# Performance work log

Measured on AMD Instinct MI355X. Metric: run time of the kernel, lower is better.

Reference implementation:

```python
import jax, jax.numpy as jnp
import numpy as np

N_NODES = 100000
N_EDGES = 3200000
DIMS = [9, 18, 54, 108]


def setup_inputs() -> dict:
    key = jax.random.key(0)
    ks = jax.random.split(key, 10)
    inp = {
        "x": jax.random.normal(ks[0], (N_NODES, DIMS[0]), dtype=jnp.float32),
        "edge_index": jax.random.randint(ks[1], (2, N_EDGES), 0, N_NODES, dtype=jnp.int64),
        "edge_weight": jax.random.uniform(ks[2], (N_EDGES,), dtype=jnp.float32),
    }
    # Glorot-ish init for GCN weights, zero bias (PyG default bias init is zeros)
    for i in range(3):
        fan_in, fan_out = DIMS[i], DIMS[i + 1]
        s = (6.0 / (fan_in + fan_out)) ** 0.5
        inp[f"W{i+1}"] = jax.random.uniform(ks[3 + i], (fan_in, fan_out), jnp.float32, -s, s)
        inp[f"b{i+1}"] = jnp.zeros((fan_out,), dtype=jnp.float32)
    return inp


def _gcn_norm(edge_index, edge_weight, n_nodes):
    # Add self loops with weight 1, then symmetric normalization (PyG gcn_norm).
    loop = jnp.arange(n_nodes, dtype=edge_index.dtype)
    src = jnp.concatenate([edge_index[0], loop])
    dst = jnp.concatenate([edge_index[1], loop])
    w = jnp.concatenate([edge_weight, jnp.ones((n_nodes,), edge_weight.dtype)])
    deg = jax.ops.segment_sum(w, dst, num_segments=n_nodes)  # [N]
    dis = jnp.where(deg > 0, jax.lax.rsqrt(jnp.where(deg > 0, deg, 1.0)), 0.0)
    norm = dis[src] * w * dis[dst]  # [E+N]
    return src, dst, norm


def _gcn_layer(x, W, b, src, dst, norm, n_nodes):
    h = x @ W                              # [N, out] small GEMM
    msg = h[src] * norm[:, None]           # gather + scale  [E+N, out]
    out = jax.ops.segment_sum(msg, dst, num_segments=n_nodes)  # scatter-add
    return out + b


def reference(x, edge_index, edge_weight, W1, b1, W2, b2, W3, b3):
    n = x.shape[0]
    src, dst, norm = _gcn_norm(edge_index, edge_weight, n)
    h = jax.nn.relu(_gcn_layer(x, W1, b1, src, dst, norm, n))
    h = jax.nn.relu(_gcn_layer(h, W2, b2, src, dst, norm, n))
    h = jax.nn.relu(_gcn_layer(h, W3, b3, src, dst, norm, n))
    return h
```

## Files before the change

kernel.cpp:

```cpp
#include <hip/hip_runtime.h>
#include <hip/hip_fp16.h>

#define NN 100000
#define NE 3200000
#define NB 391
#define BCAP 9216
#define EPB 8192

static inline int cdiv(long long a, int b) { return (int)((a + b - 1) / b); }

__global__ __launch_bounds__(1024) void k_scatterB(
    const int* __restrict__ dst, const int* __restrict__ src, const float* __restrict__ w,
    int* __restrict__ bsize, int2* __restrict__ barr) {
    __shared__ int hcnt[NB];
    __shared__ int hbase[NB];
    int t = threadIdx.x;
    for (int b = t; b < NB; b += 1024) hcnt[b] = 0;
    __syncthreads();
    int base = blockIdx.x * EPB;
    int cd[8];
#pragma unroll
    for (int k = 0; k < 8; ++k) {
        int e = base + t + (k << 10);
        cd[k] = (e < NE) ? dst[e] : -1;
        if (cd[k] >= 0) atomicAdd(&hcnt[cd[k] >> 8], 1);
    }
    __syncthreads();
    for (int b = t; b < NB; b += 1024) {
        int c = hcnt[b];
        hbase[b] = (c > 0) ? atomicAdd(&bsize[b], c) : 0;
    }
    __syncthreads();
    for (int b = t; b < NB; b += 1024) hcnt[b] = 0;
    __syncthreads();
#pragma unroll
    for (int k = 0; k < 8; ++k) {
        int e = base + t + (k << 10);
        if (cd[k] >= 0) {
            int d = cd[k];
            int bk = d >> 8;
            int rk = atomicAdd(&hcnt[bk], 1);
            int pos = hbase[bk] + rk;
            if (pos < BCAP) {
                int key = ((d & 255) << 17) | src[e];
                barr[(size_t)bk * BCAP + pos] = make_int2(key, __float_as_int(w[e]));
            }
        }
    }
}

__global__ void k_scanBB(const int* __restrict__ bsize, int* __restrict__ bbase) {
    __shared__ int s[512];
    int t = threadIdx.x;
    int v = (t < NB) ? bsize[t] : 0;
    s[t] = v;
    __syncthreads();
    for (int d = 1; d < 512; d <<= 1) {
        int a = (t >= d) ? s[t - d] : 0;
        __syncthreads();
        s[t] += a;
        __syncthreads();
    }
    if (t < NB) bbase[t] = s[t] - v;
}

__global__ __launch_bounds__(256) void k_bucketCSR(
    const int2* __restrict__ barr, const int* __restrict__ bsize, const int* __restrict__ bbase,
    int* __restrict__ rowptr, float* __restrict__ dis, unsigned int* __restrict__ e2,
    const float* __restrict__ x, __half* __restrict__ y1) {
    __shared__ int cnt[256];
    __shared__ float wsum[256];
    __shared__ int rbase[256];
    __shared__ int sc[256];
    int b = blockIdx.x;
    int t = threadIdx.x;
    int nE = bsize[b];
    int ebase = bbase[b];
    const int2* rec = barr + (size_t)b * BCAP;
    cnt[t] = 0;
    wsum[t] = 0.0f;
    __syncthreads();
    for (int e = t; e < nE; e += 256) {
        int2 r = rec[e];
        int dl = (r.x >> 17) & 255;
        atomicAdd(&cnt[dl], 1);
        atomicAdd(&wsum[dl], __int_as_float(r.y));
    }
    __syncthreads();
    int v = cnt[t];
    sc[t] = v;
    __syncthreads();
    for (int d = 1; d < 256; d <<= 1) {
        int a = (t >= d) ? sc[t - d] : 0;
        __syncthreads();
        sc[t] += a;
        __syncthreads();
    }
    rbase[t] = sc[t] - v;
    int node = (b << 8) + t;
    float disv = rsqrtf(1.0f + wsum[t]);
    if (node < NN) {
        rowptr[node] = ebase + rbase[t];
        dis[node] = disv;
    }
    if (node == NN) rowptr[NN] = ebase + rbase[t];
    cnt[t] = 0;
    wsum[t] = disv;
    __syncthreads();
    for (int e = t; e < nE; e += 256) {
        int2 r = rec[e];
        int dl = (r.x >> 17) & 255;
        int rk = atomicAdd(&cnt[dl], 1);
        float wv = __int_as_float(r.y);
        int q = (int)(wv * 32768.0f + 0.5f);
        q = (q > 32767) ? 32767 : q;
        e2[(size_t)(ebase + rbase[dl] + rk)] = ((unsigned int)(r.x & 0x1FFFF) << 15) | (unsigned int)q;
    }
    int nbase = b << 8;
#pragma unroll
    for (int k = 0; k < 9; ++k) {
        int idx = (k << 8) + t;
        if (idx < 2304) {
            int nl = idx / 9;
            int f = idx - nl * 9;
            int nd = nbase + nl;
            if (nd < NN)
                y1[(size_t)nd * 16 + f] = __float2half(x[(size_t)nd * 9 + f] * wsum[nl]);
        }
    }
}

template <int F, int FPL, int YS>
__global__ void k_agg3h(const __half* __restrict__ yin, const float* __restrict__ dis,
                        const int* __restrict__ rowptr, const unsigned int* __restrict__ e2,
                        float* __restrict__ agg, int n) {
    constexpr int LPN = F / FPL;
    constexpr int NPW = 64 / LPN;
    int wv = threadIdx.x >> 6;
    int l = threadIdx.x & 63;
    int ni = l / LPN;
    int sub = l - ni * LPN;
    if (ni >= NPW) return;
    int i = (blockIdx.x * 4 + wv) * NPW + ni;
    if (i >= n) return;

    float acc0, acc1;
    if (FPL == 2) {
        __half2 hs = *(const __half2*)(yin + (size_t)i * YS + sub * 2);
        acc0 = __low2float(hs);
        acc1 = __high2float(hs);
    } else {
        acc0 = __half2float(yin[(size_t)i * YS + sub]);
        acc1 = 0.0f;
    }

    int e0 = rowptr[i];
    int e1 = rowptr[i + 1];
    int e = e0;
    const float QS = 1.0f / 32768.0f;
    for (; e + 8 <= e1; e += 8) {
        unsigned int r[8];
#pragma unroll
        for (int k = 0; k < 8; ++k) r[k] = e2[e + k];
        if (FPL == 2) {
            __half2 h[8];
#pragma unroll
            for (int k = 0; k < 8; ++k)
                h[k] = *(const __half2*)(yin + (size_t)(r[k] >> 15) * YS + sub * 2);
#pragma unroll
            for (int k = 0; k < 8; ++k) {
                float wq = (float)(r[k] & 32767u) * QS;
                acc0 = fmaf(__low2float(h[k]), wq, acc0);
                acc1 = fmaf(__high2float(h[k]), wq, acc1);
            }
        } else {
            float hv[8];
#pragma unroll
            for (int k = 0; k < 8; ++k)
                hv[k] = __half2float(yin[(size_t)(r[k] >> 15) * YS + sub]);
#pragma unroll
            for (int k = 0; k < 8; ++k) {
                float wq = (float)(r[k] & 32767u) * QS;
                acc0 = fmaf(hv[k], wq, acc0);
            }
        }
    }
    for (; e < e1; ++e) {
        unsigned int r = e2[e];
        float wq = (float)(r & 32767u) * QS;
        if (FPL == 2) {
            __half2 h = *(const __half2*)(yin + (size_t)(r >> 15) * YS + sub * 2);
            acc0 = fmaf(__low2float(h), wq, acc0);
            acc1 = fmaf(__high2float(h), wq, acc1);
        } else {
            acc0 = fmaf(__half2float(yin[(size_t)(r >> 15) * YS + sub]), wq, acc0);
        }
    }

    float di = dis[i];
    float* orow = agg + (size_t)i * F + sub * FPL;
    if (FPL == 2) {
        *(float2*)orow = make_float2(acc0 * di, acc1 * di);
    } else {
        orow[0] = acc0 * di;
    }
}

template <int FIN, int FOUT, int OSPLIT, int OS, bool SCALE, bool HALF_OUT>
__global__ __launch_bounds__(256) void k_gemm4(
    const float* __restrict__ agg, const float* __restrict__ W,
    const float* __restrict__ bias, const float* __restrict__ dis,
    void* __restrict__ outp, int n) {
    constexpr int CH = FOUT / OSPLIT;
    constexpr int NGRP = 4 / OSPLIT;
    int wv = threadIdx.x >> 6;
    int l = threadIdx.x & 63;
    int j = __builtin_amdgcn_readfirstlane(wv & (OSPLIT - 1));
    int grp = wv >> ((OSPLIT == 4) ? 2 : (OSPLIT == 2) ? 1 : 0);
    int i = (blockIdx.x * NGRP + grp) * 64 + l;
    if (i >= n) return;

    float row[FIN];
    const float* arow = agg + (size_t)i * FIN;
#pragma unroll
    for (int f = 0; f < FIN; ++f) row[f] = arow[f];
    float sc = SCALE ? dis[i] : 1.0f;
    const float* Wj = W + j * CH;
    const float* bj = bias + j * CH;
    float acc[CH];
#pragma unroll
    for (int jj = 0; jj < CH; ++jj) acc[jj] = bj[jj];
#pragma unroll
    for (int f = 0; f < FIN; ++f) {
#pragma unroll
        for (int jj = 0; jj < CH; ++jj)
            acc[jj] = fmaf(row[f], Wj[f * FOUT + jj], acc[jj]);
    }
    if (HALF_OUT) {
        __half* orow = (__half*)outp + (size_t)i * OS + j * CH;
#pragma unroll
        for (int jj = 0; jj < CH; ++jj)
            orow[jj] = __float2half(fmaxf(acc[jj], 0.0f) * sc);
    } else {
        float* orow = (float*)outp + (size_t)i * OS + j * CH;
#pragma unroll
        for (int jj = 0; jj < CH; ++jj) orow[jj] = fmaxf(acc[jj], 0.0f) * sc;
    }
}

extern "C" void kernel_launch(void* const* d_in, const int* in_sizes, int n_in,
                              void* d_out, int out_size, void* d_ws, size_t ws_size,
                              hipStream_t stream) {
    const float* x  = (const float*)d_in[0];
    const int*   ei = (const int*)d_in[1];
    const float* ew = (const float*)d_in[2];
    const float* W1 = (const float*)d_in[3];
    const float* b1 = (const float*)d_in[4];
    const float* W2 = (const float*)d_in[5];
    const float* b2 = (const float*)d_in[6];
    const float* W3 = (const float*)d_in[7];
    const float* b3 = (const float*)d_in[8];
    float* out = (float*)d_out;

    const int* src = ei;
    const int* dst = ei + NE;

    char* ws = (char*)d_ws;
    size_t off = 0;
    auto alloc = [&](size_t bytes) {
        char* p = ws + off;
        off += (bytes + 511) / 512 * 512;
        return p;
    };
    float*        dis    = (float*)alloc((size_t)NN * 4);
    int*          rowptr = (int*)alloc((size_t)(NN + 1) * 4);
    int*          bsize  = (int*)alloc(NB * 4);
    int*          bbase  = (int*)alloc(NB * 4);
    unsigned int* e2     = (unsigned int*)alloc((size_t)NE * 4);
    float*        bufA   = (float*)alloc((size_t)NN * 54 * 4);
    __half*       y2     = (__half*)alloc((size_t)NN * 32 * 2);
    __half*       y3     = (__half*)alloc((size_t)NN * 64 * 2);
    __half*       y1     = (__half*)alloc((size_t)NN * 16 * 2);

    int2* barr = (int2*)bufA;

    const int B = 256;

    hipMemsetAsync(bsize, 0, NB * 4, stream);
    k_scatterB<<<cdiv(NE, EPB), 1024, 0, stream>>>(dst, src, ew, bsize, barr);
    k_scanBB<<<1, 512, 0, stream>>>(bsize, bbase);
    k_bucketCSR<<<NB, B, 0, stream>>>(barr, bsize, bbase, rowptr, dis, e2, x, y1);

    const int NPB9  = (64 / 9) * 4;
    const int NPB18 = (64 / (18 / 2)) * 4;
    const int NPB54 = (64 / (54 / 2)) * 4;

    k_agg3h<9, 1, 16><<<cdiv(NN, NPB9), B, 0, stream>>>(y1, dis, rowptr, e2, bufA, NN);
    k_gemm4<9, 18, 2, 32, true, true><<<cdiv(NN, 128), B, 0, stream>>>(bufA, W1, b1, dis, y2, NN);

    k_agg3h<18, 2, 32><<<cdiv(NN, NPB18), B, 0, stream>>>(y2, dis, rowptr, e2, bufA, NN);
    k_gemm4<18, 54, 2, 64, true, true><<<cdiv(NN, 128), B, 0, stream>>>(bufA, W2, b2, dis, y3, NN);

    k_agg3h<54, 2, 64><<<cdiv(NN, NPB54), B, 0, stream>>>(y3, dis, rowptr, e2, bufA, NN);
    k_gemm4<54, 108, 4, 108, false, false><<<cdiv(NN, 64), B, 0, stream>>>(bufA, W3, b3, dis, out, NN);
}
```

Before: 277.7 us.

## Widen aggregation to 4 features per lane with padded strides; enlarge CSR blocks

The aggregation kernel now has each lane gather 4 half-precision features with one 8-byte load instead of 1 or 2, so more nodes fit in each wavefront. The intermediate agg buffer gets padded row strides (12/20/56), and the GEMM kernel takes a separate input stride to match. The bucket-CSR build kernel moves from 256 to 1024 threads per block, with the per-node phases guarded to the first 256 threads. The aim is fewer gather instructions per edge and more memory-level parallelism. The cost is padding lanes that read and write unused feature slots and a larger agg buffer footprint.

```diff
diff --git a/kernel.cpp b/kernel.cpp
--- a/kernel.cpp
+++ b/kernel.cpp
@@ -64,7 +64,7 @@
     if (t < NB) bbase[t] = s[t] - v;
 }
 
-__global__ __launch_bounds__(256) void k_bucketCSR(
+__global__ __launch_bounds__(1024) void k_bucketCSR(
     const int2* __restrict__ barr, const int* __restrict__ bsize, const int* __restrict__ bbase,
     int* __restrict__ rowptr, float* __restrict__ dis, unsigned int* __restrict__ e2,
     const float* __restrict__ x, __half* __restrict__ y1) {
@@ -77,37 +77,38 @@
     int nE = bsize[b];
     int ebase = bbase[b];
     const int2* rec = barr + (size_t)b * BCAP;
-    cnt[t] = 0;
-    wsum[t] = 0.0f;
-    __syncthreads();
-    for (int e = t; e < nE; e += 256) {
+    if (t < 256) { cnt[t] = 0; wsum[t] = 0.0f; }
+    __syncthreads();
+    for (int e = t; e < nE; e += 1024) {
         int2 r = rec[e];
         int dl = (r.x >> 17) & 255;
         atomicAdd(&cnt[dl], 1);
         atomicAdd(&wsum[dl], __int_as_float(r.y));
     }
     __syncthreads();
-    int v = cnt[t];
-    sc[t] = v;
+    int v = 0;
+    if (t < 256) { v = cnt[t]; sc[t] = v; }
     __syncthreads();
     for (int d = 1; d < 256; d <<= 1) {
-        int a = (t >= d) ? sc[t - d] : 0;
-        __syncthreads();
-        sc[t] += a;
-        __syncthreads();
-    }
-    rbase[t] = sc[t] - v;
-    int node = (b << 8) + t;
-    float disv = rsqrtf(1.0f + wsum[t]);
-    if (node < NN) {
-        rowptr[node] = ebase + rbase[t];
-        dis[node] = disv;
-    }
-    if (node == NN) rowptr[NN] = ebase + rbase[t];
-    cnt[t] = 0;
-    wsum[t] = disv;
-    __syncthreads();
-    for (int e = t; e < nE; e += 256) {
+        int a = (t >= d && t < 256) ? sc[t - d] : 0;
+        __syncthreads();
+        if (t < 256) sc[t] += a;
+        __syncthreads();
+    }
+    if (t < 256) {
+        rbase[t] = sc[t] - v;
+        int node = (b << 8) + t;
+        float disv = rsqrtf(1.0f + wsum[t]);
+        if (node < NN) {
+            rowptr[node] = ebase + rbase[t];
+            dis[node] = disv;
+        }
+        if (node == NN) rowptr[NN] = ebase + rbase[t];
+        cnt[t] = 0;
+        wsum[t] = disv;
+    }
+    __syncthreads();
+    for (int e = t; e < nE; e += 1024) {
         int2 r = rec[e];
         int dl = (r.x >> 17) & 255;
         int rk = atomicAdd(&cnt[dl], 1);
@@ -118,8 +119,8 @@
     }
     int nbase = b << 8;
 #pragma unroll
-    for (int k = 0; k < 9; ++k) {
-        int idx = (k << 8) + t;
+    for (int k = 0; k < 3; ++k) {
+        int idx = (k << 10) + t;
         if (idx < 2304) {
             int nl = idx / 9;
             int f = idx - nl * 9;
@@ -130,11 +131,10 @@
     }
 }
 
-template <int F, int FPL, int YS>
-__global__ void k_agg3h(const __half* __restrict__ yin, const float* __restrict__ dis,
-                        const int* __restrict__ rowptr, const unsigned int* __restrict__ e2,
-                        float* __restrict__ agg, int n) {
-    constexpr int LPN = F / FPL;
+template <int LPN, int YS, int OS>
+__global__ void k_agg4(const __half* __restrict__ yin, const float* __restrict__ dis,
+                       const int* __restrict__ rowptr, const unsigned int* __restrict__ e2,
+                       float* __restrict__ agg, int n) {
     constexpr int NPW = 64 / LPN;
     int wv = threadIdx.x >> 6;
     int l = threadIdx.x & 63;
@@ -144,14 +144,13 @@
     int i = (blockIdx.x * 4 + wv) * NPW + ni;
     if (i >= n) return;
 
-    float acc0, acc1;
-    if (FPL == 2) {
-        __half2 hs = *(const __half2*)(yin + (size_t)i * YS + sub * 2);
-        acc0 = __low2float(hs);
-        acc1 = __high2float(hs);
-    } else {
-        acc0 = __half2float(yin[(size_t)i * YS + sub]);
-        acc1 = 0.0f;
+    float acc0, acc1, acc2, acc3;
+    {
+        float2 raw = *(const float2*)(yin + (size_t)i * YS + sub * 4);
+        __half2 ha = *(__half2*)&raw.x;
+        __half2 hb = *(__half2*)&raw.y;
+        acc0 = __low2float(ha); acc1 = __high2float(ha);
+        acc2 = __low2float(hb); acc3 = __high2float(hb);
     }
 
     int e0 = rowptr[i];
@@ -162,51 +161,39 @@
         unsigned int r[8];
 #pragma unroll
         for (int k = 0; k < 8; ++k) r[k] = e2[e + k];
-        if (FPL == 2) {
-            __half2 h[8];
-#pragma unroll
-            for (int k = 0; k < 8; ++k)
-                h[k] = *(const __half2*)(yin + (size_t)(r[k] >> 15) * YS + sub * 2);
-#pragma unroll
-            for (int k = 0; k < 8; ++k) {
-                float wq = (float)(r[k] & 32767u) * QS;
-                acc0 = fmaf(__low2float(h[k]), wq, acc0);
-                acc1 = fmaf(__high2float(h[k]), wq, acc1);
-            }
-        } else {
-            float hv[8];
-#pragma unroll
-            for (int k = 0; k < 8; ++k)
-                hv[k] = __half2float(yin[(size_t)(r[k] >> 15) * YS + sub]);
-#pragma unroll
-            for (int k = 0; k < 8; ++k) {
-                float wq = (float)(r[k] & 32767u) * QS;
-                acc0 = fmaf(hv[k], wq, acc0);
-            }
+        float2 raw[8];
+#pragma unroll
+        for (int k = 0; k < 8; ++k)
+            raw[k] = *(const float2*)(yin + (size_t)(r[k] >> 15) * YS + sub * 4);
+#pragma unroll
+        for (int k = 0; k < 8; ++k) {
+            float wq = (float)(r[k] & 32767u) * QS;
+            __half2 ha = *(__half2*)&raw[k].x;
+            __half2 hb = *(__half2*)&raw[k].y;
+            acc0 = fmaf(__low2float(ha), wq, acc0);
+            acc1 = fmaf(__high2float(ha), wq, acc1);
+            acc2 = fmaf(__low2float(hb), wq, acc2);
+            acc3 = fmaf(__high2float(hb), wq, acc3);
         }
     }
     for (; e < e1; ++e) {
         unsigned int r = e2[e];
         float wq = (float)(r & 32767u) * QS;
-        if (FPL == 2) {
-            __half2 h = *(const __half2*)(yin + (size_t)(r >> 15) * YS + sub * 2);
-            acc0 = fmaf(__low2float(h), wq, acc0);
-            acc1 = fmaf(__high2float(h), wq, acc1);
-        } else {
-            acc0 = fmaf(__half2float(yin[(size_t)(r >> 15) * YS + sub]), wq, acc0);
-        }
+        float2 raw = *(const float2*)(yin + (size_t)(r >> 15) * YS + sub * 4);
+        __half2 ha = *(__half2*)&raw.x;
+        __half2 hb = *(__half2*)&raw.y;
+        acc0 = fmaf(__low2float(ha), wq, acc0);
+        acc1 = fmaf(__high2float(ha), wq, acc1);
+        acc2 = fmaf(__low2float(hb), wq, acc2);
+        acc3 = fmaf(__high2float(hb), wq, acc3);
     }
 
     float di = dis[i];
-    float* orow = agg + (size_t)i * F + sub * FPL;
-    if (FPL == 2) {
-        *(float2*)orow = make_float2(acc0 * di, acc1 * di);
-    } else {
-        orow[0] = acc0 * di;
-    }
-}
-
-template <int FIN, int FOUT, int OSPLIT, int OS, bool SCALE, bool HALF_OUT>
+    float4* orow = (float4*)(agg + (size_t)i * OS + sub * 4);
+    *orow = make_float4(acc0 * di, acc1 * di, acc2 * di, acc3 * di);
+}
+
+template <int FIN, int IS, int FOUT, int OSPLIT, int OS, bool SCALE, bool HALF_OUT>
 __global__ __launch_bounds__(256) void k_gemm4(
     const float* __restrict__ agg, const float* __restrict__ W,
     const float* __restrict__ bias, const float* __restrict__ dis,
@@ -221,7 +208,7 @@
     if (i >= n) return;
 
     float row[FIN];
-    const float* arow = agg + (size_t)i * FIN;
+    const float* arow = agg + (size_t)i * IS;
 #pragma unroll
     for (int f = 0; f < FIN; ++f) row[f] = arow[f];
     float sc = SCALE ? dis[i] : 1.0f;
@@ -277,7 +264,7 @@
     int*          bsize  = (int*)alloc(NB * 4);
     int*          bbase  = (int*)alloc(NB * 4);
     unsigned int* e2     = (unsigned int*)alloc((size_t)NE * 4);
-    float*        bufA   = (float*)alloc((size_t)NN * 54 * 4);
+    float*        bufA   = (float*)alloc((size_t)NN * 56 * 4);
     __half*       y2     = (__half*)alloc((size_t)NN * 32 * 2);
     __half*       y3     = (__half*)alloc((size_t)NN * 64 * 2);
     __half*       y1     = (__half*)alloc((size_t)NN * 16 * 2);
@@ -289,18 +276,18 @@
     hipMemsetAsync(bsize, 0, NB * 4, stream);
     k_scatterB<<<cdiv(NE, EPB), 1024, 0, stream>>>(dst, src, ew, bsize, barr);
     k_scanBB<<<1, 512, 0, stream>>>(bsize, bbase);
-    k_bucketCSR<<<NB, B, 0, stream>>>(barr, bsize, bbase, rowptr, dis, e2, x, y1);
-
-    const int NPB9  = (64 / 9) * 4;
-    const int NPB18 = (64 / (18 / 2)) * 4;
-    const int NPB54 = (64 / (54 / 2)) * 4;
-
-    k_agg3h<9, 1, 16><<<cdiv(NN, NPB9), B, 0, stream>>>(y1, dis, rowptr, e2, bufA, NN);
-    k_gemm4<9, 18, 2, 32, true, true><<<cdiv(NN, 128), B, 0, stream>>>(bufA, W1, b1, dis, y2, NN);
-
-    k_agg3h<18, 2, 32><<<cdiv(NN, NPB18), B, 0, stream>>>(y2, dis, rowptr, e2, bufA, NN);
-    k_gemm4<18, 54, 2, 64, true, true><<<cdiv(NN, 128), B, 0, stream>>>(bufA, W2, b2, dis, y3, NN);
-
-    k_agg3h<54, 2, 64><<<cdiv(NN, NPB54), B, 0, stream>>>(y3, dis, rowptr, e2, bufA, NN);
-    k_gemm4<54, 108, 4, 108, false, false><<<cdiv(NN, 64), B, 0, stream>>>(bufA, W3, b3, dis, out, NN);
-}
+    k_bucketCSR<<<NB, 1024, 0, stream>>>(barr, bsize, bbase, rowptr, dis, e2, x, y1);
+
+    const int NPB9  = (64 / 3) * 4;
+    const int NPB18 = (64 / 5) * 4;
+    const int NPB54 = (64 / 14) * 4;
+
+    k_agg4<3, 16, 12><<<cdiv(NN, NPB9), B, 0, stream>>>(y1, dis, rowptr, e2, bufA, NN);
+    k_gemm4<9, 12, 18, 2, 32, true, true><<<cdiv(NN, 128), B, 0, stream>>>(bufA, W1, b1, dis, y2, NN);
+
+    k_agg4<5, 32, 20><<<cdiv(NN, NPB18), B, 0, stream>>>(y2, dis, rowptr, e2, bufA, NN);
+    k_gemm4<18, 20, 54, 2, 64, true, true><<<cdiv(NN, 128), B, 0, stream>>>(bufA, W2, b2, dis, y3, NN);
+
+    k_agg4<14, 64, 56><<<cdiv(NN, NPB54), B, 0, stream>>>(y3, dis, rowptr, e2, bufA, NN);
+    k_gemm4<54, 56, 108, 4, 108, false, false><<<cdiv(NN, 64), B, 0, stream>>>(bufA, W3, b3, dis, out, NN);
+}
```

After: 267.6 us. 3.6% less time.
